# Optimization experiments

Measured on AMD Instinct MI355X. Metric: run time of the kernel, lower is better.

## Reference

```python
import math
import jax, jax.numpy as jnp
import numpy as np

R, N, B, E, H, M = 128, 256, 1, 512, 8, 4
D = E // H
NEG = -1e9  # eye-mask fill value from masked_fill(-1000000000)


def setup_inputs() -> dict:
    key = jax.random.key(0)
    ks = jax.random.split(key, 10)
    p = lambda k, shape: jax.random.normal(k, shape, jnp.float32) * 0.02
    z = lambda n: jnp.zeros((n,), jnp.float32)
    return {
        "x": jax.random.normal(ks[0], (R, N, B, E), jnp.float32),
        "network": jax.random.uniform(ks[1], (B, N, N, M), jnp.float32),
        "Wq": p(ks[2], (E, E)), "bq": z(E),
        "Wk": p(ks[3], (E, E)), "bk": z(E),
        "Wv": p(ks[4], (E, E)), "bv": z(E),
        "Wo": p(ks[5], (E, E)), "bo": z(E),
        "Wq1": p(ks[6], (D, 8)), "bq1": z(8),
        "Wk1": p(ks[7], (1, 8)), "bk1": z(8),
        "l": jax.random.normal(ks[8], (H, 1, 1, 1), jnp.float32),
    }


def reference(x, network, Wq, bq, Wk, bk, Wv, bv, Wo, bo, Wq1, bq1, Wk1, bk1, l):
    # x: [R, N, B, E]; network: [B, N, N, M] (B must be 1, as in the torch module)
    scaling = (D ** -0.5) / math.sqrt(R)  # align_scaling

    q = (x @ Wq + bq).reshape(R, N, B, H, D) * scaling
    k = (x @ Wk + bk).reshape(R, N, B, H, D)

    # shared contraction: summed over rows r, kept per head-dim d -> [H, B, N, N, D]
    qk = jnp.einsum('rinhd,rjnhd->hnijd', q, k)

    # network-bias MLP branch
    q1 = (qk @ Wq1 + bq1).mean(0)                  # [B, N, N, 8]
    network_k = network[..., None] * Wk1[0] + bk1  # Linear(1,8): [B, N, N, M, 8]
    net_attn = jnp.einsum('nijd,nijmd->nijm', q1, network_k)  # [B, N, N, M]
    net_attn = jnp.tile(net_attn, (H, 1, 1, 1))    # repeat over heads (B==1) -> [H, N, N, M]

    # attn_weights 'rinhd,rjnhd->hnij' == qk summed over d
    attn_weights = qk.sum(-1)                      # [H, B, N, N]

    net_probs = jax.nn.softmax(net_attn, axis=-1)  # softmax over M network channels
    net_bias = (network * net_probs).sum(-1)[:, None, :, :]  # [H, 1(B), N, N]
    attn_weights = attn_weights + l * net_bias

    eye = jnp.eye(N, dtype=bool)
    attn_weights = jnp.where(eye, NEG, attn_weights)
    attn_probs = jax.nn.softmax(attn_weights, axis=-1)  # [H, B, N, N]

    v = (x @ Wv + bv).reshape(R, N, B, H, D)
    context = jnp.einsum('hnij,rjnhd->rinhd', attn_probs, v).reshape(R, N, B, E)
    output = context @ Wo + bo
    return (output, attn_probs, l)
```

## Files before the change

kernel.cpp:

```cpp
#include <hip/hip_runtime.h>
#include <hip/hip_bf16.h>
#include <cmath>
#include <stdint.h>

using bf16 = __hip_bfloat16;
typedef __attribute__((ext_vector_type(8))) short bf16x8;
typedef __attribute__((ext_vector_type(4))) float f32x4;

constexpr long HS = 2097152;

__device__ __forceinline__ void gload16(const bf16* g, bf16* l)
{
  __builtin_amdgcn_global_load_lds(
      (const __attribute__((address_space(1))) void*)g,
      (__attribute__((address_space(3))) void*)l,
      16, 0, 0);
}

__device__ __forceinline__ int swsrc(int c) { return (((c & 3) ^ ((c >> 3) & 3)) * 8); }

__global__ __launch_bounds__(256)
void k_convert_x(const float* __restrict__ x, bf16* __restrict__ xb)
{
  const long idx = (long)blockIdx.x * 256 + threadIdx.x;
  const float4 f0 = *(const float4*)&x[idx * 8];
  const float4 f1 = *(const float4*)&x[idx * 8 + 4];
  alignas(16) bf16 t[8] = {
    __float2bfloat16(f0.x), __float2bfloat16(f0.y),
    __float2bfloat16(f0.z), __float2bfloat16(f0.w),
    __float2bfloat16(f1.x), __float2bfloat16(f1.y),
    __float2bfloat16(f1.z), __float2bfloat16(f1.w)};
  *(uint4*)&xb[idx * 8] = *(const uint4*)t;
}

__global__ __launch_bounds__(256)
void k_prep_w(const float* __restrict__ Wq, const float* __restrict__ Wk,
              const float* __restrict__ Wv, const float* __restrict__ Wo,
              bf16* __restrict__ WT, float scaling)
{
  const int sel = blockIdx.z;
  const float* W = sel == 0 ? Wq : sel == 1 ? Wk : sel == 2 ? Wv : Wo;
  const float sc = sel == 0 ? scaling : 1.0f;
  const int k0 = blockIdx.x * 64, n0 = blockIdx.y * 64;
  __shared__ float tile[64][68];
  const int tid = threadIdx.x;
  #pragma unroll
  for (int it = 0; it < 4; it++) {
    const int c = tid + it * 256;
    const int kk = c >> 4, nn4 = (c & 15) * 4;
    const float4 v = *(const float4*)&W[(long)(k0 + kk) * 512 + n0 + nn4];
    tile[kk][nn4] = v.x; tile[kk][nn4 + 1] = v.y;
    tile[kk][nn4 + 2] = v.z; tile[kk][nn4 + 3] = v.w;
  }
  __syncthreads();
  #pragma unroll
  for (int it = 0; it < 2; it++) {
    const int c = tid + it * 256;
    const int nn = c >> 3, k8 = (c & 7) * 8;
    alignas(16) bf16 t[8];
    #pragma unroll
    for (int jj = 0; jj < 8; jj++) t[jj] = __float2bfloat16(tile[k8 + jj][nn] * sc);
    *(uint4*)&WT[(long)(sel * 512 + n0 + nn) * 512 + k0 + k8] = *(const uint4*)t;
  }
}

__global__ void k_prep_small(const float* __restrict__ bq, const float* __restrict__ bk,
                             const float* __restrict__ bv, const float* __restrict__ bo,
                             const float* __restrict__ Wq1, const float* __restrict__ Wk1,
                             float* __restrict__ bias_all, float* __restrict__ u, float scaling)
{
  const int idx = blockIdx.x * 256 + threadIdx.x;
  const int s2 = idx >> 9, n2 = idx & 511;
  const float* b = s2 == 0 ? bq : s2 == 1 ? bk : s2 == 2 ? bv : bo;
  bias_all[idx] = b[n2] * (s2 == 0 ? scaling : 1.0f);
  if (idx < 64) {
    float s = 0.0f;
    #pragma unroll
    for (int c = 0; c < 8; c++) s += Wq1[idx * 8 + c] * Wk1[c];
    u[idx] = s;
  }
}

__global__ __launch_bounds__(512, 2)
void gemm_qkv(const bf16* __restrict__ xb, const bf16* __restrict__ WT,
              const float* __restrict__ bias_all,
              bf16* __restrict__ Qn, bf16* __restrict__ Kn, bf16* __restrict__ Vj)
{
  __shared__ __align__(16) unsigned short smem[65536];
  bf16* As = (bf16*)smem;
  bf16* Bs = (bf16*)smem + 32768;
  const int tid = threadIdx.x, lane = tid & 63;
  const int wid = tid >> 6, wr = wid >> 2, wc = wid & 3;
  const int lr = lane & 15;
  const int lkx = ((lane >> 4) ^ ((lane >> 1) & 3)) * 8;
  const int flat = ((int)blockIdx.x & 7) * 96 + ((int)blockIdx.x >> 3);
  const int m0 = (flat / 6) * 256, nt = flat % 6, n0 = nt * 256;
  const int c1 = tid + 512;
  const int ra0 = tid >> 2, ra1 = c1 >> 2;
  const int ps0 = swsrc(tid), ps1 = swsrc(c1);
  f32x4 acc[8][4] = {};

  auto stage = [&](int b, int k0) {
    gload16(&xb[(long)(m0 + ra0) * 512 + k0 + ps0], &As[b * 8192 + tid * 8]);
    gload16(&xb[(long)(m0 + ra1) * 512 + k0 + ps1], &As[b * 8192 + c1 * 8]);
    gload16(&WT[(long)(n0 + ra0) * 512 + k0 + ps0], &Bs[b * 8192 + tid * 8]);
    gload16(&WT[(long)(n0 + ra1) * 512 + k0 + ps1], &Bs[b * 8192 + c1 * 8]);
  };

  stage(0, 0);
  stage(1, 32);
  stage(2, 64);

  for (int t = 0; t < 16; ++t) {
    const int cur = t & 3;
    if (t < 13) stage((t + 3) & 3, (t + 3) * 32);
    if (t == 0) {
      asm volatile("s_waitcnt vmcnt(12)" ::: "memory");
      __builtin_amdgcn_s_barrier();
    }
    bf16x8 af[8], bfr[4];
    #pragma unroll
    for (int n = 0; n < 4; n++)
      bfr[n] = *(const bf16x8*)&Bs[cur * 8192 + (wc * 64 + n * 16 + lr) * 32 + lkx];
    #pragma unroll
    for (int m = 0; m < 8; m++)
      af[m] = *(const bf16x8*)&As[cur * 8192 + (wr * 128 + m * 16 + lr) * 32 + lkx];
    __builtin_amdgcn_s_setprio(1);
    #pragma unroll
    for (int m = 0; m < 8; m++)
      #pragma unroll
      for (int n = 0; n < 4; n++)
        acc[m][n] = __builtin_amdgcn_mfma_f32_16x16x32_bf16(af[m], bfr[n], acc[m][n], 0, 0, 0);
    __builtin_amdgcn_s_setprio(0);
    if (t < 13)       asm volatile("s_waitcnt vmcnt(8)" ::: "memory");
    else if (t == 13) asm volatile("s_waitcnt vmcnt(4)" ::: "memory");
    else if (t == 14) asm volatile("s_waitcnt vmcnt(0)" ::: "memory");
    __builtin_amdgcn_s_barrier();
  }

  const int er = (lane >> 4) * 4, ec = lane & 15;
  if (nt < 4) {
    bf16* dst = (nt < 2) ? Qn : Kn;
    const int cb = (nt < 2) ? n0 : n0 - 512;
    #pragma unroll
    for (int m = 0; m < 8; m++) {
      const int row0 = m0 + wr * 128 + m * 16 + er;
      #pragma unroll
      for (int n = 0; n < 4; n++) {
        const int cw = wc * 64 + n * 16 + ec;
        const float bv = bias_all[n0 + cw];
        #pragma unroll
        for (int q = 0; q < 4; q++)
          dst[(long)(row0 + q) * 512 + cb + cw] = __float2bfloat16(acc[m][n][q] + bv);
      }
    }
  } else {
    bf16* vt = (bf16*)smem;
    const int r = m0 >> 8;
    const int hdbase = (nt - 4) * 256;
    #pragma unroll 1
    for (int p = 0; p < 4; ++p) {
      __syncthreads();
      if (wc == p) {
        #pragma unroll
        for (int m = 0; m < 8; m++) {
          const int rt0 = wr * 128 + m * 16 + er;
          #pragma unroll
          for (int n = 0; n < 4; n++) {
            const int ct = n * 16 + ec;
            const float bv = bias_all[n0 + p * 64 + ct];
            #pragma unroll
            for (int q = 0; q < 4; q++)
              vt[ct * 264 + rt0 + q] = __float2bfloat16(acc[m][n][q] + bv);
          }
        }
      }
      __syncthreads();
      #pragma unroll
      for (int cc = 0; cc < 4; cc++) {
        const int c = cc * 512 + tid;
        const int hl = c >> 5, tok8 = (c & 31) * 8;
        const uint4 v = *(const uint4*)&vt[hl * 264 + tok8];
        const int hd = hdbase + p * 64 + hl;
        const int h = hd >> 6, d = hd & 63;
        *(uint4*)&Vj[(long)h * HS + (long)(r * 64 + d) * 256 + tok8] = v;
      }
    }
  }
}

__global__ __launch_bounds__(256)
void gemm_logits(const bf16* __restrict__ Qn, const bf16* __restrict__ Kn,
                 const float* __restrict__ u, float* __restrict__ part)
{
  __shared__ bf16 As[4][128 * 32];
  __shared__ bf16 Bs[4][128 * 32];
  __shared__ float us[64];
  const int tid = threadIdx.x, lane = tid & 63;
  const int wid = tid >> 6, wr = wid >> 1, wc = wid & 1;
  const int lr = lane & 15;
  const int lkx = ((lane >> 4) ^ ((lane >> 1) & 3)) * 8;
  const int z = blockIdx.z, batch = z >> 2, ks = z & 3, h = batch & 7;
  const bool uscale = batch >= 8;
  const int m0 = blockIdx.y * 128, n0 = blockIdx.x * 128;
  if (tid < 64) us[tid] = u[tid];
  __syncthreads();
  float ufa[8], ufb[8];
  const int gbase = (lane >> 4) * 8;
  #pragma unroll
  for (int j = 0; j < 8; j++) { ufa[j] = us[gbase + j]; ufb[j] = us[32 + gbase + j]; }
  const int c1 = tid + 256;
  const int ra0 = tid >> 2, ra1 = c1 >> 2;
  const int ps = swsrc(tid);
  f32x4 acc[4][4] = {};

  auto stage = [&](int b, int kk) {
    const int gk = ks * 2048 + kk * 32;
    const int r = gk >> 6, d0 = gk & 63;
    const long ab = (long)(r * 256 + m0) * 512 + h * 64 + d0;
    const long bb = (long)(r * 256 + n0) * 512 + h * 64 + d0;
    gload16(&Qn[ab + (long)ra0 * 512 + ps], &As[b][tid * 8]);
    gload16(&Qn[ab + (long)ra1 * 512 + ps], &As[b][c1 * 8]);
    gload16(&Kn[bb + (long)ra0 * 512 + ps], &Bs[b][tid * 8]);
    gload16(&Kn[bb + (long)ra1 * 512 + ps], &Bs[b][c1 * 8]);
  };

  stage(0, 0);
  stage(1, 1);
  stage(2, 2);

  for (int kk = 0; kk < 64; ++kk) {
    const int cur = kk & 3;
    if (kk < 61) stage((kk + 3) & 3, kk + 3);
    if (kk == 0) {
      asm volatile("s_waitcnt vmcnt(12)" ::: "memory");
      __builtin_amdgcn_s_barrier();
    }
    bf16x8 af[4], bfr[4];
    #pragma unroll
    for (int m = 0; m < 4; m++)
      af[m] = *(const bf16x8*)&As[cur][(wr * 64 + m * 16 + lr) * 32 + lkx];
    #pragma unroll
    for (int n = 0; n < 4; n++)
      bfr[n] = *(const bf16x8*)&Bs[cur][(wc * 64 + n * 16 + lr) * 32 + lkx];
    if (uscale) {
      const bool odd = (kk & 1) != 0;
      #pragma unroll
      for (int m = 0; m < 4; m++) {
        #pragma unroll
        for (int j = 0; j < 8; j++) {
          const unsigned short a_ = (unsigned short)af[m][j];
          const float f = __bfloat162float(*(const bf16*)&a_) * (odd ? ufb[j] : ufa[j]);
          const bf16 b_ = __float2bfloat16(f);
          af[m][j] = *(const short*)&b_;
        }
      }
    }
    __builtin_amdgcn_s_setprio(1);
    #pragma unroll
    for (int m = 0; m < 4; m++)
      #pragma unroll
      for (int n = 0; n < 4; n++)
        acc[m][n] = __builtin_amdgcn_mfma_f32_16x16x32_bf16(af[m], bfr[n], acc[m][n], 0, 0, 0);
    __builtin_amdgcn_s_setprio(0);
    if (kk < 61)       asm volatile("s_waitcnt vmcnt(8)" ::: "memory");
    else if (kk == 61) asm volatile("s_waitcnt vmcnt(4)" ::: "memory");
    else if (kk == 62) asm volatile("s_waitcnt vmcnt(0)" ::: "memory");
    __builtin_amdgcn_s_barrier();
  }

  float* C = part + (long)z * 65536;
  const int er = (lane >> 4) * 4, ec = lane & 15;
  #pragma unroll
  for (int m = 0; m < 4; m++)
    #pragma unroll
    for (int n = 0; n < 4; n++) {
      const int col = n0 + wc * 64 + n * 16 + ec;
      #pragma unroll
      for (int q = 0; q < 4; q++)
        C[(long)(m0 + wr * 64 + m * 16 + er + q) * 256 + col] = acc[m][n][q];
    }
}

__global__ __launch_bounds__(256)
void gemm_ctx(const bf16* __restrict__ Pb, const bf16* __restrict__ Vj,
              bf16* __restrict__ ctxb)
{
  __shared__ bf16 As[3][128 * 32];
  __shared__ bf16 Bs[3][128 * 32];
  const int tid = threadIdx.x, lane = tid & 63;
  const int wid = tid >> 6, wr = wid >> 1, wc = wid & 1;
  const int lr = lane & 15;
  const int lkx = ((lane >> 4) ^ ((lane >> 1) & 3)) * 8;
  const int m0 = blockIdx.y * 128, n0 = blockIdx.x * 128, h = blockIdx.z;
  const bf16* A = Pb + (long)h * 65536;
  const bf16* B = Vj + (long)h * HS;
  const int c1 = tid + 256;
  const int ra0 = tid >> 2, ra1 = c1 >> 2;
  const int ps = swsrc(tid);
  f32x4 acc[4][4] = {};

  auto stage = [&](int b, int k0) {
    gload16(&A[(long)(m0 + ra0) * 256 + k0 + ps], &As[b][tid * 8]);
    gload16(&A[(long)(m0 + ra1) * 256 + k0 + ps], &As[b][c1 * 8]);
    gload16(&B[(long)(n0 + ra0) * 256 + k0 + ps], &Bs[b][tid * 8]);
    gload16(&B[(long)(n0 + ra1) * 256 + k0 + ps], &Bs[b][c1 * 8]);
  };

  stage(0, 0);
  stage(1, 32);

  for (int t = 0; t < 8; ++t) {
    const int cur = t % 3;
    if (t < 6) {
      stage((t + 2) % 3, (t + 2) * 32);
      asm volatile("s_waitcnt vmcnt(8)" ::: "memory");
    } else if (t == 6) {
      asm volatile("s_waitcnt vmcnt(4)" ::: "memory");
    } else {
      asm volatile("s_waitcnt vmcnt(0)" ::: "memory");
    }
    __builtin_amdgcn_s_barrier();
    bf16x8 af[4], bfr[4];
    #pragma unroll
    for (int m = 0; m < 4; m++)
      af[m] = *(const bf16x8*)&As[cur][(wr * 64 + m * 16 + lr) * 32 + lkx];
    #pragma unroll
    for (int n = 0; n < 4; n++)
      bfr[n] = *(const bf16x8*)&Bs[cur][(wc * 64 + n * 16 + lr) * 32 + lkx];
    #pragma unroll
    for (int m = 0; m < 4; m++)
      #pragma unroll
      for (int n = 0; n < 4; n++)
        acc[m][n] = __builtin_amdgcn_mfma_f32_16x16x32_bf16(af[m], bfr[n], acc[m][n], 0, 0, 0);
    __builtin_amdgcn_s_barrier();
  }

  const int er = (lane >> 4) * 4, ec = lane & 15;
  #pragma unroll
  for (int m = 0; m < 4; m++) {
    const int i0 = m0 + wr * 64 + m * 16 + er;
    #pragma unroll
    for (int n = 0; n < 4; n++) {
      const int col = n0 + wc * 64 + n * 16 + ec;
      const int rr = col >> 6, dd = col & 63;
      #pragma unroll
      for (int q = 0; q < 4; q++)
        ctxb[(long)(rr * 256 + i0 + q) * 512 + h * 64 + dd] = __float2bfloat16(acc[m][n][q]);
    }
  }
}

__global__ __launch_bounds__(512)
void gemm_outp(const bf16* __restrict__ A, const bf16* __restrict__ B,
               float* __restrict__ C, const float* __restrict__ bias)
{
  __shared__ bf16 As[3][128 * 32];
  __shared__ bf16 Bs[3][256 * 32];
  const int tid = threadIdx.x, lane = tid & 63, wid = tid >> 6;
  const int wr = wid >> 2, wc = wid & 3;
  const int lr = lane & 15;
  const int lkx = ((lane >> 4) ^ ((lane >> 1) & 3)) * 8;
  const int m0 = blockIdx.y * 128, n0 = blockIdx.x * 256;
  const int ra = tid >> 2;
  const int cb1 = tid + 512;
  const int rb0 = tid >> 2, rb1 = cb1 >> 2;
  const int ps = swsrc(tid);
  f32x4 acc[4][4] = {};

  auto stage = [&](int b, int k0) {
    gload16(&A[(long)(m0 + ra) * 512 + k0 + ps], &As[b][tid * 8]);
    gload16(&B[(long)(n0 + rb0) * 512 + k0 + ps], &Bs[b][tid * 8]);
    gload16(&B[(long)(n0 + rb1) * 512 + k0 + ps], &Bs[b][cb1 * 8]);
  };

  stage(0, 0);
  stage(1, 32);

  for (int t = 0; t < 16; ++t) {
    const int cur = t % 3;
    if (t < 14) {
      stage((t + 2) % 3, (t + 2) * 32);
      asm volatile("s_waitcnt vmcnt(6)" ::: "memory");
    } else if (t == 14) {
      asm volatile("s_waitcnt vmcnt(3)" ::: "memory");
    } else {
      asm volatile("s_waitcnt vmcnt(0)" ::: "memory");
    }
    __builtin_amdgcn_s_barrier();
    bf16x8 af[4], bfr[4];
    #pragma unroll
    for (int m = 0; m < 4; m++)
      af[m] = *(const bf16x8*)&As[cur][(wr * 64 + m * 16 + lr) * 32 + lkx];
    #pragma unroll
    for (int n = 0; n < 4; n++)
      bfr[n] = *(const bf16x8*)&Bs[cur][(wc * 64 + n * 16 + lr) * 32 + lkx];
    #pragma unroll
    for (int m = 0; m < 4; m++)
      #pragma unroll
      for (int n = 0; n < 4; n++)
        acc[m][n] = __builtin_amdgcn_mfma_f32_16x16x32_bf16(af[m], bfr[n], acc[m][n], 0, 0, 0);
    __builtin_amdgcn_s_barrier();
  }

  const int er = (lane >> 4) * 4, ec = lane & 15;
  #pragma unroll
  for (int m = 0; m < 4; m++) {
    const int row0 = m0 + wr * 64 + m * 16 + er;
    #pragma unroll
    for (int n = 0; n < 4; n++) {
      const int col = n0 + wc * 64 + n * 16 + ec;
      const float bv = bias[col];
      #pragma unroll
      for (int q = 0; q < 4; q++)
        C[(long)(row0 + q) * 512 + col] = acc[m][n][q] + bv;
    }
  }
}

__global__ void k_bias(const float* __restrict__ part, const float* __restrict__ network,
                       const float* __restrict__ bq1, const float* __restrict__ Wk1,
                       float* __restrict__ net_bias)
{
  const int i = blockIdx.x, j = threadIdx.x;
  float c1 = 0.0f;
  #pragma unroll
  for (int c = 0; c < 8; c++) c1 += bq1[c] * Wk1[c];
  float s1 = 0.0f;
  const long ij = i * 256 + j;
  #pragma unroll
  for (int s = 32; s < 64; s++) s1 += part[(long)s * 65536 + ij];
  s1 = 0.125f * s1 + c1;
  const float4 nw = *(const float4*)&network[ij * 4];
  const float a0 = nw.x * s1, a1 = nw.y * s1, a2 = nw.z * s1, a3 = nw.w * s1;
  const float mx = fmaxf(fmaxf(a0, a1), fmaxf(a2, a3));
  const float e0 = expf(a0 - mx), e1 = expf(a1 - mx), e2 = expf(a2 - mx), e3 = expf(a3 - mx);
  const float inv = 1.0f / (e0 + e1 + e2 + e3);
  net_bias[ij] = (nw.x * e0 + nw.y * e1 + nw.z * e2 + nw.w * e3) * inv;
}

__global__ void k_softmax(const float* __restrict__ part, const float* __restrict__ net_bias,
                          const float* __restrict__ l, float* __restrict__ out_probs,
                          bf16* __restrict__ Pb, float* __restrict__ out_l)
{
  const int i = blockIdx.x, h = blockIdx.y, j = threadIdx.x;
  const long ij = i * 256 + j;
  float w = 0.0f;
  #pragma unroll
  for (int ks = 0; ks < 4; ks++) w += part[(long)(h * 4 + ks) * 65536 + ij];
  w += l[h] * net_bias[ij];
  if (j == i) w = -1e9f;
  float m = w;
  #pragma unroll
  for (int o = 32; o; o >>= 1) m = fmaxf(m, __shfl_xor(m, o));
  __shared__ float red[4], red2[4];
  if ((j & 63) == 0) red[j >> 6] = m;
  __syncthreads();
  m = fmaxf(fmaxf(red[0], red[1]), fmaxf(red[2], red[3]));
  const float e = expf(w - m);
  float s = e;
  #pragma unroll
  for (int o = 32; o; o >>= 1) s += __shfl_xor(s, o);
  if ((j & 63) == 0) red2[j >> 6] = s;
  __syncthreads();
  s = red2[0] + red2[1] + red2[2] + red2[3];
  const float p = e / s;
  out_probs[(long)h * 65536 + ij] = p;
  Pb[(long)h * 65536 + ij] = __float2bfloat16(p);
  if (h == 0 && i == 0 && j < 8) out_l[j] = l[j];
}

extern "C" void kernel_launch(void* const* d_in, const int* in_sizes, int n_in,
                              void* d_out, int out_size, void* d_ws, size_t ws_size,
                              hipStream_t stream)
{
  const float* x   = (const float*)d_in[0];
  const float* net = (const float*)d_in[1];
  const float* Wq  = (const float*)d_in[2];
  const float* bq  = (const float*)d_in[3];
  const float* Wk  = (const float*)d_in[4];
  const float* bk  = (const float*)d_in[5];
  const float* Wv  = (const float*)d_in[6];
  const float* bv  = (const float*)d_in[7];
  const float* Wo  = (const float*)d_in[8];
  const float* bo  = (const float*)d_in[9];
  const float* Wq1 = (const float*)d_in[10];
  const float* bq1 = (const float*)d_in[11];
  const float* Wk1 = (const float*)d_in[12];
  const float* l   = (const float*)d_in[14];
  float* out = (float*)d_out;

  bf16* Qn = (bf16*)d_out;
  bf16* Kn = Qn + 16777216;

  char* ws = (char*)d_ws;
  size_t off = 0;
  auto alloc = [&](size_t bytes) { char* p = ws + off; off += (bytes + 255) & ~255ULL; return p; };
  bf16*  WT       = (bf16*)alloc(2048ULL * 512 * 2);
  float* bias_all = (float*)alloc(2048 * 4);
  float* u        = (float*)alloc(64 * 4);
  bf16*  xb       = (bf16*)alloc(16777216ULL * 2);
  bf16*  Vj       = (bf16*)alloc(16777216ULL * 2);
  float* net_bias = (float*)alloc(65536ULL * 4);
  bf16*  Pb       = (bf16*)alloc(8ULL * 65536 * 2);
  float* part     = (float*)xb;
  bf16*  ctxb     = xb;

  const float scaling = (float)(0.125 / sqrt(128.0));

  k_convert_x<<<8192, 256, 0, stream>>>(x, xb);
  k_prep_w<<<dim3(8, 8, 4), 256, 0, stream>>>(Wq, Wk, Wv, Wo, WT, scaling);
  k_prep_small<<<8, 256, 0, stream>>>(bq, bk, bv, bo, Wq1, Wk1, bias_all, u, scaling);

  gemm_qkv<<<768, 512, 0, stream>>>(xb, WT, bias_all, Qn, Kn, Vj);

  gemm_logits<<<dim3(2, 2, 64), 256, 0, stream>>>(Qn, Kn, u, part);

  k_bias<<<256, 256, 0, stream>>>(part, net, bq1, Wk1, net_bias);
  k_softmax<<<dim3(256, 8, 1), 256, 0, stream>>>(part, net_bias, l,
                                                 out + 16777216, Pb, out + 17301504);

  gemm_ctx<<<dim3(64, 2, 8), 256, 0, stream>>>(Pb, Vj, ctxb);

  gemm_outp<<<dim3(2, 256, 1), 512, 0, stream>>>(ctxb, WT + 1536 * 512, out, bias_all + 1536);
}
```

Baseline: 189.9 us.

## Fuse setup and tail kernels, shrink QKV GEMM pipeline to three stages

Merges x conversion, weight transpose and bias prep into one launch, and fuses the network-bias and softmax kernels into one per-row kernel that loops over heads, removing the net_bias buffer. The QKV GEMM now uses a three-stage LDS ring instead of four and drops priority hints, reducing shared memory per block. Fewer launches and intermediate traffic are traded for less parallelism in the tail kernel and shallower prefetch in the GEMM.

```diff
diff --git a/kernel.cpp b/kernel.cpp
--- a/kernel.cpp
+++ b/kernel.cpp
@@ -20,64 +20,61 @@
 __device__ __forceinline__ int swsrc(int c) { return (((c & 3) ^ ((c >> 3) & 3)) * 8); }
 
 __global__ __launch_bounds__(256)
-void k_convert_x(const float* __restrict__ x, bf16* __restrict__ xb)
-{
-  const long idx = (long)blockIdx.x * 256 + threadIdx.x;
-  const float4 f0 = *(const float4*)&x[idx * 8];
-  const float4 f1 = *(const float4*)&x[idx * 8 + 4];
-  alignas(16) bf16 t[8] = {
-    __float2bfloat16(f0.x), __float2bfloat16(f0.y),
-    __float2bfloat16(f0.z), __float2bfloat16(f0.w),
-    __float2bfloat16(f1.x), __float2bfloat16(f1.y),
-    __float2bfloat16(f1.z), __float2bfloat16(f1.w)};
-  *(uint4*)&xb[idx * 8] = *(const uint4*)t;
-}
-
-__global__ __launch_bounds__(256)
-void k_prep_w(const float* __restrict__ Wq, const float* __restrict__ Wk,
-              const float* __restrict__ Wv, const float* __restrict__ Wo,
-              bf16* __restrict__ WT, float scaling)
-{
-  const int sel = blockIdx.z;
-  const float* W = sel == 0 ? Wq : sel == 1 ? Wk : sel == 2 ? Wv : Wo;
-  const float sc = sel == 0 ? scaling : 1.0f;
-  const int k0 = blockIdx.x * 64, n0 = blockIdx.y * 64;
+void k_setup(const float* __restrict__ x, bf16* __restrict__ xb,
+             const float* __restrict__ Wq, const float* __restrict__ Wk,
+             const float* __restrict__ Wv, const float* __restrict__ Wo,
+             const float* __restrict__ bq, const float* __restrict__ bk,
+             const float* __restrict__ bv, const float* __restrict__ bo,
+             const float* __restrict__ Wq1, const float* __restrict__ Wk1,
+             bf16* __restrict__ WT, float* __restrict__ bias_all,
+             float* __restrict__ u, float scaling)
+{
   __shared__ float tile[64][68];
-  const int tid = threadIdx.x;
-  #pragma unroll
-  for (int it = 0; it < 4; it++) {
-    const int c = tid + it * 256;
-    const int kk = c >> 4, nn4 = (c & 15) * 4;
-    const float4 v = *(const float4*)&W[(long)(k0 + kk) * 512 + n0 + nn4];
-    tile[kk][nn4] = v.x; tile[kk][nn4 + 1] = v.y;
-    tile[kk][nn4 + 2] = v.z; tile[kk][nn4 + 3] = v.w;
-  }
-  __syncthreads();
-  #pragma unroll
-  for (int it = 0; it < 2; it++) {
-    const int c = tid + it * 256;
-    const int nn = c >> 3, k8 = (c & 7) * 8;
-    alignas(16) bf16 t[8];
-    #pragma unroll
-    for (int jj = 0; jj < 8; jj++) t[jj] = __float2bfloat16(tile[k8 + jj][nn] * sc);
-    *(uint4*)&WT[(long)(sel * 512 + n0 + nn) * 512 + k0 + k8] = *(const uint4*)t;
-  }
-}
-
-__global__ void k_prep_small(const float* __restrict__ bq, const float* __restrict__ bk,
-                             const float* __restrict__ bv, const float* __restrict__ bo,
-                             const float* __restrict__ Wq1, const float* __restrict__ Wk1,
-                             float* __restrict__ bias_all, float* __restrict__ u, float scaling)
-{
-  const int idx = blockIdx.x * 256 + threadIdx.x;
-  const int s2 = idx >> 9, n2 = idx & 511;
-  const float* b = s2 == 0 ? bq : s2 == 1 ? bk : s2 == 2 ? bv : bo;
-  bias_all[idx] = b[n2] * (s2 == 0 ? scaling : 1.0f);
-  if (idx < 64) {
-    float s = 0.0f;
-    #pragma unroll
-    for (int c = 0; c < 8; c++) s += Wq1[idx * 8 + c] * Wk1[c];
-    u[idx] = s;
+  const int bid = blockIdx.x, tid = threadIdx.x;
+  if (bid < 8192) {
+    const long idx = (long)bid * 256 + tid;
+    const float4 f0 = *(const float4*)&x[idx * 8];
+    const float4 f1 = *(const float4*)&x[idx * 8 + 4];
+    alignas(16) bf16 t[8] = {
+      __float2bfloat16(f0.x), __float2bfloat16(f0.y),
+      __float2bfloat16(f0.z), __float2bfloat16(f0.w),
+      __float2bfloat16(f1.x), __float2bfloat16(f1.y),
+      __float2bfloat16(f1.z), __float2bfloat16(f1.w)};
+    *(uint4*)&xb[idx * 8] = *(const uint4*)t;
+  } else if (bid < 8448) {
+    const int b2 = bid - 8192;
+    const int sel = b2 >> 6, k0 = (b2 & 7) * 64, n0 = ((b2 >> 3) & 7) * 64;
+    const float* W = sel == 0 ? Wq : sel == 1 ? Wk : sel == 2 ? Wv : Wo;
+    const float sc = sel == 0 ? scaling : 1.0f;
+    #pragma unroll
+    for (int it = 0; it < 4; it++) {
+      const int c = tid + it * 256;
+      const int kk = c >> 4, nn4 = (c & 15) * 4;
+      const float4 v = *(const float4*)&W[(long)(k0 + kk) * 512 + n0 + nn4];
+      tile[kk][nn4] = v.x; tile[kk][nn4 + 1] = v.y;
+      tile[kk][nn4 + 2] = v.z; tile[kk][nn4 + 3] = v.w;
+    }
+    __syncthreads();
+    #pragma unroll
+    for (int it = 0; it < 2; it++) {
+      const int c = tid + it * 256;
+      const int nn = c >> 3, k8 = (c & 7) * 8;
+      alignas(16) bf16 t[8];
+      #pragma unroll
+      for (int jj = 0; jj < 8; jj++) t[jj] = __float2bfloat16(tile[k8 + jj][nn] * sc);
+      *(uint4*)&WT[(long)(sel * 512 + n0 + nn) * 512 + k0 + k8] = *(const uint4*)t;
+    }
+  } else {
+    const int idx = (bid - 8448) * 256 + tid;
+    const int s2 = idx >> 9, n2 = idx & 511;
+    const float* b = s2 == 0 ? bq : s2 == 1 ? bk : s2 == 2 ? bv : bo;
+    bias_all[idx] = b[n2] * (s2 == 0 ? scaling : 1.0f);
+    if (idx < 64) {
+      float s = 0.0f;
+      #pragma unroll
+      for (int c = 0; c < 8; c++) s += Wq1[idx * 8 + c] * Wk1[c];
+      u[idx] = s;
+    }
   }
 }
 
@@ -86,9 +83,9 @@
               const float* __restrict__ bias_all,
               bf16* __restrict__ Qn, bf16* __restrict__ Kn, bf16* __restrict__ Vj)
 {
-  __shared__ __align__(16) unsigned short smem[65536];
+  __shared__ __align__(16) unsigned short smem[49152];
   bf16* As = (bf16*)smem;
-  bf16* Bs = (bf16*)smem + 32768;
+  bf16* Bs = (bf16*)smem + 24576;
   const int tid = threadIdx.x, lane = tid & 63;
   const int wid = tid >> 6, wr = wid >> 2, wc = wid & 3;
   const int lr = lane & 15;
@@ -109,13 +106,12 @@
 
   stage(0, 0);
   stage(1, 32);
-  stage(2, 64);
 
   for (int t = 0; t < 16; ++t) {
-    const int cur = t & 3;
-    if (t < 13) stage((t + 3) & 3, (t + 3) * 32);
+    const int cur = t % 3;
+    if (t < 14) stage((t + 2) % 3, (t + 2) * 32);
     if (t == 0) {
-      asm volatile("s_waitcnt vmcnt(12)" ::: "memory");
+      asm volatile("s_waitcnt vmcnt(8)" ::: "memory");
       __builtin_amdgcn_s_barrier();
     }
     bf16x8 af[8], bfr[4];
@@ -125,15 +121,12 @@
     #pragma unroll
     for (int m = 0; m < 8; m++)
       af[m] = *(const bf16x8*)&As[cur * 8192 + (wr * 128 + m * 16 + lr) * 32 + lkx];
-    __builtin_amdgcn_s_setprio(1);
     #pragma unroll
     for (int m = 0; m < 8; m++)
       #pragma unroll
       for (int n = 0; n < 4; n++)
         acc[m][n] = __builtin_amdgcn_mfma_f32_16x16x32_bf16(af[m], bfr[n], acc[m][n], 0, 0, 0);
-    __builtin_amdgcn_s_setprio(0);
-    if (t < 13)       asm volatile("s_waitcnt vmcnt(8)" ::: "memory");
-    else if (t == 13) asm volatile("s_waitcnt vmcnt(4)" ::: "memory");
+    if (t < 14)       asm volatile("s_waitcnt vmcnt(4)" ::: "memory");
     else if (t == 14) asm volatile("s_waitcnt vmcnt(0)" ::: "memory");
     __builtin_amdgcn_s_barrier();
   }
@@ -283,6 +276,57 @@
 }
 
 __global__ __launch_bounds__(256)
+void k_tail(const float* __restrict__ part, const float* __restrict__ network,
+            const float* __restrict__ bq1, const float* __restrict__ Wk1,
+            const float* __restrict__ l, float* __restrict__ out_probs,
+            bf16* __restrict__ Pb, float* __restrict__ out_l)
+{
+  const int i = blockIdx.x, j = threadIdx.x;
+  const long ij = i * 256 + j;
+  __shared__ float red[4], red2[4];
+
+  float c1 = 0.0f;
+  #pragma unroll
+  for (int c = 0; c < 8; c++) c1 += bq1[c] * Wk1[c];
+  float s1 = 0.0f;
+  #pragma unroll
+  for (int s = 32; s < 64; s++) s1 += part[(long)s * 65536 + ij];
+  s1 = 0.125f * s1 + c1;
+  const float4 nw = *(const float4*)&network[ij * 4];
+  const float a0 = nw.x * s1, a1 = nw.y * s1, a2 = nw.z * s1, a3 = nw.w * s1;
+  const float mx0 = fmaxf(fmaxf(a0, a1), fmaxf(a2, a3));
+  const float e0 = expf(a0 - mx0), e1 = expf(a1 - mx0), e2 = expf(a2 - mx0), e3 = expf(a3 - mx0);
+  const float nb = (nw.x * e0 + nw.y * e1 + nw.z * e2 + nw.w * e3) / (e0 + e1 + e2 + e3);
+
+  #pragma unroll 1
+  for (int h = 0; h < 8; h++) {
+    float w = 0.0f;
+    #pragma unroll
+    for (int ks = 0; ks < 4; ks++) w += part[(long)(h * 4 + ks) * 65536 + ij];
+    w += l[h] * nb;
+    if (j == i) w = -1e9f;
+    float m = w;
+    #pragma unroll
+    for (int o = 32; o; o >>= 1) m = fmaxf(m, __shfl_xor(m, o));
+    if ((j & 63) == 0) red[j >> 6] = m;
+    __syncthreads();
+    m = fmaxf(fmaxf(red[0], red[1]), fmaxf(red[2], red[3]));
+    const float e = expf(w - m);
+    float s = e;
+    #pragma unroll
+    for (int o = 32; o; o >>= 1) s += __shfl_xor(s, o);
+    if ((j & 63) == 0) red2[j >> 6] = s;
+    __syncthreads();
+    s = red2[0] + red2[1] + red2[2] + red2[3];
+    const float p = e / s;
+    out_probs[(long)h * 65536 + ij] = p;
+    Pb[(long)h * 65536 + ij] = __float2bfloat16(p);
+    __syncthreads();
+  }
+  if (i == 0 && j < 8) out_l[j] = l[j];
+}
+
+__global__ __launch_bounds__(256)
 void gemm_ctx(const bf16* __restrict__ Pb, const bf16* __restrict__ Vj,
               bf16* __restrict__ ctxb)
 {
@@ -416,58 +460,6 @@
         C[(long)(row0 + q) * 512 + col] = acc[m][n][q] + bv;
     }
   }
-}
-
-__global__ void k_bias(const float* __restrict__ part, const float* __restrict__ network,
-                       const float* __restrict__ bq1, const float* __restrict__ Wk1,
-                       float* __restrict__ net_bias)
-{
-  const int i = blockIdx.x, j = threadIdx.x;
-  float c1 = 0.0f;
-  #pragma unroll
-  for (int c = 0; c < 8; c++) c1 += bq1[c] * Wk1[c];
-  float s1 = 0.0f;
-  const long ij = i * 256 + j;
-  #pragma unroll
-  for (int s = 32; s < 64; s++) s1 += part[(long)s * 65536 + ij];
-  s1 = 0.125f * s1 + c1;
-  const float4 nw = *(const float4*)&network[ij * 4];
-  const float a0 = nw.x * s1, a1 = nw.y * s1, a2 = nw.z * s1, a3 = nw.w * s1;
-  const float mx = fmaxf(fmaxf(a0, a1), fmaxf(a2, a3));
-  const float e0 = expf(a0 - mx), e1 = expf(a1 - mx), e2 = expf(a2 - mx), e3 = expf(a3 - mx);
-  const float inv = 1.0f / (e0 + e1 + e2 + e3);
-  net_bias[ij] = (nw.x * e0 + nw.y * e1 + nw.z * e2 + nw.w * e3) * inv;
-}
-
-__global__ void k_softmax(const float* __restrict__ part, const float* __restrict__ net_bias,
-                          const float* __restrict__ l, float* __restrict__ out_probs,
-                          bf16* __restrict__ Pb, float* __restrict__ out_l)
-{
-  const int i = blockIdx.x, h = blockIdx.y, j = threadIdx.x;
-  const long ij = i * 256 + j;
-  float w = 0.0f;
-  #pragma unroll
-  for (int ks = 0; ks < 4; ks++) w += part[(long)(h * 4 + ks) * 65536 + ij];
-  w += l[h] * net_bias[ij];
-  if (j == i) w = -1e9f;
-  float m = w;
-  #pragma unroll
-  for (int o = 32; o; o >>= 1) m = fmaxf(m, __shfl_xor(m, o));
-  __shared__ float red[4], red2[4];
-  if ((j & 63) == 0) red[j >> 6] = m;
-  __syncthreads();
-  m = fmaxf(fmaxf(red[0], red[1]), fmaxf(red[2], red[3]));
-  const float e = expf(w - m);
-  float s = e;
-  #pragma unroll
-  for (int o = 32; o; o >>= 1) s += __shfl_xor(s, o);
-  if ((j & 63) == 0) red2[j >> 6] = s;
-  __syncthreads();
-  s = red2[0] + red2[1] + red2[2] + red2[3];
-  const float p = e / s;
-  out_probs[(long)h * 65536 + ij] = p;
-  Pb[(long)h * 65536 + ij] = __float2bfloat16(p);
-  if (h == 0 && i == 0 && j < 8) out_l[j] = l[j];
 }
 
 extern "C" void kernel_launch(void* const* d_in, const int* in_sizes, int n_in,
@@ -501,24 +493,21 @@
   float* u        = (float*)alloc(64 * 4);
   bf16*  xb       = (bf16*)alloc(16777216ULL * 2);
   bf16*  Vj       = (bf16*)alloc(16777216ULL * 2);
-  float* net_bias = (float*)alloc(65536ULL * 4);
   bf16*  Pb       = (bf16*)alloc(8ULL * 65536 * 2);
   float* part     = (float*)xb;
   bf16*  ctxb     = xb;
 
   const float scaling = (float)(0.125 / sqrt(128.0));
 
-  k_convert_x<<<8192, 256, 0, stream>>>(x, xb);
-  k_prep_w<<<dim3(8, 8, 4), 256, 0, stream>>>(Wq, Wk, Wv, Wo, WT, scaling);
-  k_prep_small<<<8, 256, 0, stream>>>(bq, bk, bv, bo, Wq1, Wk1, bias_all, u, scaling);
+  k_setup<<<8456, 256, 0, stream>>>(x, xb, Wq, Wk, Wv, Wo, bq, bk, bv, bo,
+                                    Wq1, Wk1, WT, bias_all, u, scaling);
 
   gemm_qkv<<<768, 512, 0, stream>>>(xb, WT, bias_all, Qn, Kn, Vj);
 
   gemm_logits<<<dim3(2, 2, 64), 256, 0, stream>>>(Qn, Kn, u, part);
 
-  k_bias<<<256, 256, 0, stream>>>(part, net, bq1, Wk1, net_bias);
-  k_softmax<<<dim3(256, 8, 1), 256, 0, stream>>>(part, net_bias, l,
-                                                 out + 16777216, Pb, out + 17301504);
+  k_tail<<<256, 256, 0, stream>>>(part, net, bq1, Wk1, l,
+                                  out + 16777216, Pb, out + 17301504);
 
   gemm_ctx<<<dim3(64, 2, 8), 256, 0, stream>>>(Pb, Vj, ctxb);
 
```

Result: no change. 189.6 us (-0.2%).
